# Kernel optimization log

Measured on AMD Instinct MI355X. Metric: run time of the kernel, lower is better.

## Reference

```python
import jax, jax.numpy as jnp
import numpy as np


def _conv1x1_relu(x, W, b):
    # x: (B, Cin, N, k), W: (Cout, Cin), b: (Cout,) -> (B, Cout, N, k)
    return jax.nn.relu(jnp.einsum('bcnk,oc->bonk', x, W) + b[None, :, None, None])


def _knn_idx(pc, k):
    # pc: (B, C, N). Mirrors torch: dis_mat = -||pi - pj||^2, topk (largest) -> nearest.
    G = jnp.einsum('bcn,bcm->bnm', pc, pc)            # (B, N, N)
    sq = jnp.sum(pc * pc, axis=1)                      # (B, N)
    neg_dist = 2.0 * G - sq[:, :, None] - sq[:, None, :]
    _, idx = jax.lax.top_k(neg_dist, k)                # (B, N, k) int32
    return idx


def _group_points(x, idx):
    # x: (B, C, N), idx: (B, N, k) -> (B, C, N, k); out[b,c,n,j] = x[b,c,idx[b,n,j]]
    B, C, N = x.shape
    k = idx.shape[-1]
    idx2 = jnp.broadcast_to(idx.reshape(B, 1, N * k), (B, C, N * k))
    return jnp.take_along_axis(x, idx2, axis=2).reshape(B, C, N, k)


def setup_inputs() -> dict:
    key = jax.random.key(0)
    ks = jax.random.split(key, 8)
    B, N, C, O, K = 8, 4096, 64, 64, 16
    s = 0.05
    return {
        'xyz': jax.random.normal(ks[0], (B, 3, N), dtype=jnp.float32),
        'fea': jax.random.normal(ks[1], (B, C, N), dtype=jnp.float32),
        'Wg1': jax.random.normal(ks[2], (O, 10), dtype=jnp.float32) * s,
        'bg1': jnp.zeros((O,), dtype=jnp.float32),
        'Wg2': jax.random.normal(ks[3], (O, O), dtype=jnp.float32) * s,
        'bg2': jnp.zeros((O,), dtype=jnp.float32),
        'Wf1': jax.random.normal(ks[4], (O, 2 * C), dtype=jnp.float32) * s,
        'bf1': jnp.zeros((O,), dtype=jnp.float32),
        'Wf2': jax.random.normal(ks[5], (O, O), dtype=jnp.float32) * s,
        'bf2': jnp.zeros((O,), dtype=jnp.float32),
        'Wf3': jax.random.normal(ks[6], (O, O), dtype=jnp.float32) * s,
        'bf3': jnp.zeros((O,), dtype=jnp.float32),
        'k': 16,
    }


def reference(xyz, fea, Wg1, bg1, Wg2, bg2, Wf1, bf1, Wf2, bf2, Wf3, bf3, k):
    idx = _knn_idx(fea, k)                             # (B, N, k)

    # get_edge_point: (B, 10, N, k)
    xyz_knn = _group_points(xyz, idx)                  # (B, 3, N, k)
    xyz_c = jnp.broadcast_to(xyz[:, :, :, None], xyz_knn.shape)
    xyz_r = xyz_c - xyz_knn
    xyz_d = jnp.sqrt(jnp.sum(xyz_r * xyz_r, axis=1, keepdims=True))
    geo = jnp.concatenate([xyz_d, xyz_c, xyz_knn, xyz_r], axis=1)

    # get_edge_feature: (B, 2C, N, k)
    fea_knn = _group_points(fea, idx)
    fea_c = jnp.broadcast_to(fea[:, :, :, None], fea_knn.shape)
    edge = jnp.concatenate([fea_c, fea_knn], axis=1)

    g = _conv1x1_relu(geo, Wg1, bg1)
    g = _conv1x1_relu(g, Wg2, bg2)

    f = _conv1x1_relu(edge, Wf1, bf1)
    f = _conv1x1_relu(f, Wf2, bf2)
    f = _conv1x1_relu(f, Wf3, bf3)

    out = jnp.max(g * f, axis=-1)                      # (B, O, N)
    return out
```

## Files before the change

kernel.cpp:

```cpp
#include <hip/hip_runtime.h>
#include <math.h>

#define NB 8
#define NPTS 4096
#define NCH 64
#define NOUT 64
#define KNN 16

#define GLOBAL_AS const __attribute__((address_space(1)))
#define LDS_AS __attribute__((address_space(3)))

#define WS_SQ  0
#define WS_PT  (NB*NPTS)
#define WS_QT  (WS_PT + NB*NPTS*64)
#define WS_IDX (WS_QT + NB*NPTS*64)

__global__ __launch_bounds__(256, 4) void k_knn(const float* __restrict__ fea,
                                                const float* __restrict__ sq,
                                                int* __restrict__ idxout) {
    __shared__ __align__(16) float rowT[64][32];
    __shared__ __align__(16) float colT[2][64 * 64];

    const int b = blockIdx.y;
    const int n0 = blockIdx.x * 32;
    const int tid = threadIdx.x;
    const int lane = tid & 63, w = tid >> 6;
    const int g = lane >> 4, p = lane & 15;
    const int rbase = w * 8 + g * 2;
    const float* feab = fea + (size_t)b * NCH * NPTS;

    auto stage = [&](int buf, int m0) {
#pragma unroll
        for (int i = 0; i < 4; ++i) {
            int k = w * 4 + i;
            int c = 4 * k + (lane >> 4);
            int j = (lane & 15) * 4;
            const float* gp = feab + c * NPTS + m0 + j;
            float* lp = &colT[buf][k * 256];
            __builtin_amdgcn_global_load_lds((GLOBAL_AS void*)gp,
                                             (LDS_AS void*)lp, 16, 0, 0);
        }
    };

#pragma unroll
    for (int i = 0; i < 2; ++i) {
        int e = i * 1024 + tid * 4;
        int c = e >> 5, r = e & 31;
        *(float4*)&rowT[c][r] = *(const float4*)&feab[c * NPTS + n0 + r];
    }

    float lstv[2];
    int   lsti[2];
    float thr[2];
#pragma unroll
    for (int i = 0; i < 2; ++i) {
        lstv[i] = -3.0e38f; lsti[i] = 0; thr[i] = -3.0e38f;
    }

    auto ins = [&](int i, float vv, int col) {
        unsigned long long lt = __ballot(lstv[i] < vv);
        int pos = __popc((unsigned)((lt >> (g * 16)) & 0xFFFFu));
        int nv = __builtin_amdgcn_update_dpp(0, __float_as_int(lstv[i]),
                                             0x101, 0xF, 0xF, true);
        int ni = __builtin_amdgcn_update_dpp(0, lsti[i],
                                             0x101, 0xF, 0xF, true);
        if (p <= pos - 2)      { lstv[i] = __int_as_float(nv); lsti[i] = ni; }
        else if (p == pos - 1) { lstv[i] = vv; lsti[i] = col; }
    };

    stage(0, 0);
    __syncthreads();

    for (int t = 0; t < 64; ++t) {
        const int m0 = t * 64;
        const int cur = t & 1;
        if (t < 63) stage(cur ^ 1, m0 + 64);

        float4 sqc = *(const float4*)&sq[b * NPTS + m0 + p * 4];

        float acc[2][4] = {{0.f,0.f,0.f,0.f},{0.f,0.f,0.f,0.f}};
#pragma unroll 8
        for (int c = 0; c < 64; ++c) {
            float2 rv = *(const float2*)&rowT[c][rbase];
            float4 cv = *(const float4*)&colT[cur][c * 64 + p * 4];
            float cc[4] = {cv.x, cv.y, cv.z, cv.w};
#pragma unroll
            for (int ci = 0; ci < 4; ++ci) {
                acc[0][ci] = fmaf(rv.x, cc[ci], acc[0][ci]);
                acc[1][ci] = fmaf(rv.y, cc[ci], acc[1][ci]);
            }
        }

        float sqa[4] = {sqc.x, sqc.y, sqc.z, sqc.w};
#pragma unroll
        for (int i = 0; i < 2; ++i)
#pragma unroll
            for (int j = 0; j < 4; ++j)
                acc[i][j] = fmaf(2.f, acc[i][j], -sqa[j]);

#pragma unroll
        for (int i = 0; i < 2; ++i) {
            float v0 = acc[i][0], v1 = acc[i][1];
            float v2 = acc[i][2], v3 = acc[i][3];
            float vm = fmaxf(fmaxf(v0, v1), fmaxf(v2, v3));
            unsigned long long bal = __ballot(vm > thr[i]);
            unsigned mg = (unsigned)((bal >> (g * 16)) & 0xFFFFull);
            while (__any(mg != 0u)) {
                bool act = (mg != 0u);
                int srcp = act ? (__ffs(mg) - 1) : 0;
                mg &= (mg - 1u);
                int srcl = (g << 4) | srcp;
                float b0 = __shfl(v0, srcl);
                float b1 = __shfl(v1, srcl);
                float b2 = __shfl(v2, srcl);
                float b3 = __shfl(v3, srcl);
                if (act) {
                    int cb = m0 + srcp * 4;
                    if (b0 > thr[i]) ins(i, b0, cb + 0);
                    if (b1 > thr[i]) ins(i, b1, cb + 1);
                    if (b2 > thr[i]) ins(i, b2, cb + 2);
                    if (b3 > thr[i]) ins(i, b3, cb + 3);
                }
            }
            if (bal) thr[i] = __shfl(lstv[i], 0, 16);
        }
        __syncthreads();
    }

#pragma unroll
    for (int i = 0; i < 2; ++i) {
        int row = rbase + i;
        idxout[((size_t)(b * NPTS) + n0 + row) * KNN + (15 - p)] = lsti[i];
    }
}

__global__ __launch_bounds__(256) void k_pq(const float* __restrict__ fea,
                                            const float* __restrict__ Wf1,
                                            const float* __restrict__ bf1,
                                            float* __restrict__ Pt,
                                            float* __restrict__ Qt,
                                            float* __restrict__ sq) {
    __shared__ __align__(16) float feaT[64][64];
    __shared__ __align__(16) float WT[64][132];
    __shared__ float sb[64];

    const int b = blockIdx.y;
    const int n0 = blockIdx.x * 64;
    const int tid = threadIdx.x;
    const int to = tid & 15, tn = tid >> 4;
    const float* feab = fea + (size_t)b * NCH * NPTS;

#pragma unroll
    for (int i = 0; i < 4; ++i) {
        int e = i * 1024 + tid * 4;
        int c = e >> 6, nn = e & 63;
        *(float4*)&feaT[c][nn] = *(const float4*)&feab[c * NPTS + n0 + nn];
    }
#pragma unroll
    for (int i = 0; i < 8; ++i) {
        int g = tid * 32 + i * 4;
        int op = g >> 6, c = g & 63;
        const float* src = (op < 64) ? &Wf1[op * 128 + c]
                                     : &Wf1[(op - 64) * 128 + 64 + c];
        float4 w = *(const float4*)src;
        WT[c + 0][op] = w.x; WT[c + 1][op] = w.y;
        WT[c + 2][op] = w.z; WT[c + 3][op] = w.w;
    }
    if (tid < 64) sb[tid] = bf1[tid];
    __syncthreads();

    if (tid < 64) {
        float s = 0.f;
#pragma unroll
        for (int c = 0; c < 64; ++c) {
            float v = feaT[c][tid];
            s = fmaf(v, v, s);
        }
        sq[b * NPTS + n0 + tid] = s;
    }

    float acc[4][8];
#pragma unroll
    for (int ni = 0; ni < 4; ++ni)
#pragma unroll
        for (int oj = 0; oj < 8; ++oj) acc[ni][oj] = 0.f;

#pragma unroll 4
    for (int c = 0; c < 64; ++c) {
        float4 a  = *(const float4*)&feaT[c][tn * 4];
        float4 w0 = *(const float4*)&WT[c][to * 8];
        float4 w1 = *(const float4*)&WT[c][to * 8 + 4];
        float av[4] = {a.x, a.y, a.z, a.w};
        float wv[8] = {w0.x, w0.y, w0.z, w0.w, w1.x, w1.y, w1.z, w1.w};
#pragma unroll
        for (int ni = 0; ni < 4; ++ni)
#pragma unroll
            for (int oj = 0; oj < 8; ++oj)
                acc[ni][oj] = fmaf(av[ni], wv[oj], acc[ni][oj]);
    }

    const int opb = to * 8;
#pragma unroll
    for (int ni = 0; ni < 4; ++ni) {
        int n = n0 + tn * 4 + ni;
        size_t base = ((size_t)b * NPTS + n) * 64;
        if (opb < 64) {
            float4 o0, o1;
            o0.x = acc[ni][0] + sb[opb + 0]; o0.y = acc[ni][1] + sb[opb + 1];
            o0.z = acc[ni][2] + sb[opb + 2]; o0.w = acc[ni][3] + sb[opb + 3];
            o1.x = acc[ni][4] + sb[opb + 4]; o1.y = acc[ni][5] + sb[opb + 5];
            o1.z = acc[ni][6] + sb[opb + 6]; o1.w = acc[ni][7] + sb[opb + 7];
            *(float4*)&Pt[base + opb]     = o0;
            *(float4*)&Pt[base + opb + 4] = o1;
        } else {
            float4 o0, o1;
            o0.x = acc[ni][0]; o0.y = acc[ni][1]; o0.z = acc[ni][2]; o0.w = acc[ni][3];
            o1.x = acc[ni][4]; o1.y = acc[ni][5]; o1.z = acc[ni][6]; o1.w = acc[ni][7];
            *(float4*)&Qt[base + opb - 64]     = o0;
            *(float4*)&Qt[base + opb - 64 + 4] = o1;
        }
    }
}

__global__ __launch_bounds__(256) void k_mlp(
    const float* __restrict__ xyz,
    const float* __restrict__ Pt, const float* __restrict__ Qt,
    const int* __restrict__ knnidx,
    const float* __restrict__ Wg1, const float* __restrict__ bg1,
    const float* __restrict__ Wg2, const float* __restrict__ bg2,
    const float* __restrict__ Wf2, const float* __restrict__ bf2,
    const float* __restrict__ Wf3, const float* __restrict__ bf3,
    float* __restrict__ out) {
    __shared__ __align__(16) float bufX[64][68];
    __shared__ __align__(16) float bufY[64][68];
    __shared__ __align__(16) float WbufA[64][68];
    __shared__ __align__(16) float WbufB[64][68];
    __shared__ __align__(16) float geoS[10 * 68];
    __shared__ float biasA[64], biasB[64];
    __shared__ int sidx[64];

    const int b = blockIdx.y;
    const int n0 = blockIdx.x * 4;
    const int tid = threadIdx.x;
    const int to = tid & 15, tp = tid >> 4;

    if (tid < 64)
        sidx[tid] = knnidx[((size_t)(b * NPTS + n0)) * KNN + tid];
    __syncthreads();

    {
        int pair = tid >> 2, q = tid & 3;
        int m = sidx[pair];
        int pt = pair >> 4;
        const float* pB = &Pt[((size_t)b * NPTS + n0 + pt) * 64];
        const float* qB = &Qt[((size_t)b * NPTS + m) * 64];
#pragma unroll
        for (int i = 0; i < 4; ++i) {
            int c0 = q * 16 + i * 4;
            float4 pv = *(const float4*)&pB[c0];
            float4 qv = *(const float4*)&qB[c0];
            bufX[c0 + 0][pair] = fmaxf(pv.x + qv.x, 0.f);
            bufX[c0 + 1][pair] = fmaxf(pv.y + qv.y, 0.f);
            bufX[c0 + 2][pair] = fmaxf(pv.z + qv.z, 0.f);
            bufX[c0 + 3][pair] = fmaxf(pv.w + qv.w, 0.f);
        }
    }
    if (tid < 64) {
        int pair = tid, pt = pair >> 4;
        int m = sidx[pair];
        const float* xb = xyz + (size_t)b * 3 * NPTS;
        float cx = xb[0 * NPTS + n0 + pt], cy = xb[1 * NPTS + n0 + pt], cz = xb[2 * NPTS + n0 + pt];
        float kx = xb[0 * NPTS + m], ky = xb[1 * NPTS + m], kz = xb[2 * NPTS + m];
        float rx = cx - kx, ry = cy - ky, rz = cz - kz;
        float d = sqrtf(rx * rx + ry * ry + rz * rz);
        geoS[0 * 68 + pair] = d;
        geoS[1 * 68 + pair] = cx; geoS[2 * 68 + pair] = cy; geoS[3 * 68 + pair] = cz;
        geoS[4 * 68 + pair] = kx; geoS[5 * 68 + pair] = ky; geoS[6 * 68 + pair] = kz;
        geoS[7 * 68 + pair] = rx; geoS[8 * 68 + pair] = ry; geoS[9 * 68 + pair] = rz;
    }

    auto stageW = [&](const float* W, const float* bv, float (*Wb)[68],
                      float* bias) {
#pragma unroll
        for (int i = 0; i < 4; ++i) {
            int g = tid * 16 + i * 4;
            int o = g >> 6, c = g & 63;
            float4 w = *(const float4*)&W[g];
            Wb[c + 0][o] = w.x; Wb[c + 1][o] = w.y;
            Wb[c + 2][o] = w.z; Wb[c + 3][o] = w.w;
        }
        if (tid < 64) bias[tid] = bv[tid];
    };

    auto gemmPh = [&](const float* src, float* dst, int Kdim,
                      const float (*Wb)[68], const float* bias) {
        float acc[4][4] = {{0.f,0.f,0.f,0.f},{0.f,0.f,0.f,0.f},
                           {0.f,0.f,0.f,0.f},{0.f,0.f,0.f,0.f}};
#pragma unroll 2
        for (int c = 0; c < Kdim; ++c) {
            float4 w = *(const float4*)&Wb[c][tp * 4];
            float4 a = *(const float4*)(src + c * 68 + to * 4);
            float wr[4] = {w.x, w.y, w.z, w.w};
            float ar[4] = {a.x, a.y, a.z, a.w};
#pragma unroll
            for (int oi = 0; oi < 4; ++oi)
#pragma unroll
                for (int pj = 0; pj < 4; ++pj)
                    acc[oi][pj] = fmaf(wr[oi], ar[pj], acc[oi][pj]);
        }
#pragma unroll
        for (int oi = 0; oi < 4; ++oi) {
            float bo = bias[tp * 4 + oi];
            float4 o4;
            o4.x = fmaxf(acc[oi][0] + bo, 0.f);
            o4.y = fmaxf(acc[oi][1] + bo, 0.f);
            o4.z = fmaxf(acc[oi][2] + bo, 0.f);
            o4.w = fmaxf(acc[oi][3] + bo, 0.f);
            *(float4*)(dst + (tp * 4 + oi) * 68 + to * 4) = o4;
        }
    };

    stageW(Wf2, bf2, WbufA, biasA);
    stageW(Wf3, bf3, WbufB, biasB);
    __syncthreads();

    gemmPh(&bufX[0][0], &bufY[0][0], 64, WbufA, biasA);
    __syncthreads();

    float f3r[4][4];
    {
        float acc[4][4] = {{0.f,0.f,0.f,0.f},{0.f,0.f,0.f,0.f},
                           {0.f,0.f,0.f,0.f},{0.f,0.f,0.f,0.f}};
#pragma unroll 2
        for (int c = 0; c < 64; ++c) {
            float4 w = *(const float4*)&WbufB[c][tp * 4];
            float4 a = *(const float4*)&bufY[c][to * 4];
            float wr[4] = {w.x, w.y, w.z, w.w};
            float ar[4] = {a.x, a.y, a.z, a.w};
#pragma unroll
            for (int oi = 0; oi < 4; ++oi)
#pragma unroll
                for (int pj = 0; pj < 4; ++pj)
                    acc[oi][pj] = fmaf(wr[oi], ar[pj], acc[oi][pj]);
        }
#pragma unroll
        for (int oi = 0; oi < 4; ++oi) {
            float bo = biasB[tp * 4 + oi];
            f3r[oi][0] = fmaxf(acc[oi][0] + bo, 0.f);
            f3r[oi][1] = fmaxf(acc[oi][1] + bo, 0.f);
            f3r[oi][2] = fmaxf(acc[oi][2] + bo, 0.f);
            f3r[oi][3] = fmaxf(acc[oi][3] + bo, 0.f);
        }
    }
    {
        for (int e = tid; e < 640; e += 256) {
            int o = e / 10, c = e - o * 10;
            WbufA[c][o] = Wg1[e];
        }
        if (tid < 64) biasA[tid] = bg1[tid];
    }
    __syncthreads();

    gemmPh(geoS, &bufY[0][0], 10, WbufA, biasA);
    stageW(Wg2, bg2, WbufB, biasB);
    __syncthreads();

    {
        float acc[4][4] = {{0.f,0.f,0.f,0.f},{0.f,0.f,0.f,0.f},
                           {0.f,0.f,0.f,0.f},{0.f,0.f,0.f,0.f}};
#pragma unroll 2
        for (int c = 0; c < 64; ++c) {
            float4 w = *(const float4*)&WbufB[c][tp * 4];
            float4 a = *(const float4*)&bufY[c][to * 4];
            float wr[4] = {w.x, w.y, w.z, w.w};
            float ar[4] = {a.x, a.y, a.z, a.w};
#pragma unroll
            for (int oi = 0; oi < 4; ++oi)
#pragma unroll
                for (int pj = 0; pj < 4; ++pj)
                    acc[oi][pj] = fmaf(wr[oi], ar[pj], acc[oi][pj]);
        }
        float mx[4];
#pragma unroll
        for (int oi = 0; oi < 4; ++oi) {
            float bo = biasB[tp * 4 + oi];
            float m0_ = fmaxf(acc[oi][0] + bo, 0.f) * f3r[oi][0];
            float m1_ = fmaxf(acc[oi][1] + bo, 0.f) * f3r[oi][1];
            float m2_ = fmaxf(acc[oi][2] + bo, 0.f) * f3r[oi][2];
            float m3_ = fmaxf(acc[oi][3] + bo, 0.f) * f3r[oi][3];
            mx[oi] = fmaxf(fmaxf(m0_, m1_), fmaxf(m2_, m3_));
        }
#pragma unroll
        for (int oi = 0; oi < 4; ++oi) {
            mx[oi] = fmaxf(mx[oi], __shfl_xor(mx[oi], 1));
            mx[oi] = fmaxf(mx[oi], __shfl_xor(mx[oi], 2));
        }
        if ((to & 3) == 0) {
            int pt = to >> 2;
#pragma unroll
            for (int oi = 0; oi < 4; ++oi) {
                int o = tp * 4 + oi;
                out[((size_t)b * 64 + o) * NPTS + n0 + pt] = mx[oi];
            }
        }
    }
}

extern "C" void kernel_launch(void* const* d_in, const int* in_sizes, int n_in,
                              void* d_out, int out_size, void* d_ws, size_t ws_size,
                              hipStream_t stream) {
    const float* xyz = (const float*)d_in[0];
    const float* fea = (const float*)d_in[1];
    const float* Wg1 = (const float*)d_in[2];
    const float* bg1 = (const float*)d_in[3];
    const float* Wg2 = (const float*)d_in[4];
    const float* bg2 = (const float*)d_in[5];
    const float* Wf1 = (const float*)d_in[6];
    const float* bf1 = (const float*)d_in[7];
    const float* Wf2 = (const float*)d_in[8];
    const float* bf2 = (const float*)d_in[9];
    const float* Wf3 = (const float*)d_in[10];
    const float* bf3 = (const float*)d_in[11];
    float* out = (float*)d_out;
    float* ws = (float*)d_ws;

    float* sq = ws + WS_SQ;
    float* Pt = ws + WS_PT;
    float* Qt = ws + WS_QT;
    int* idxw = (int*)(ws + WS_IDX);

    k_pq  <<<dim3(64, 8),    dim3(256), 0, stream>>>(fea, Wf1, bf1, Pt, Qt, sq);
    k_knn <<<dim3(128, 8),   dim3(256), 0, stream>>>(fea, sq, idxw);
    k_mlp <<<dim3(1024, 8),  dim3(256), 0, stream>>>(xyz, Pt, Qt, idxw,
                                                     Wg1, bg1, Wg2, bg2,
                                                     Wf2, bf2, Wf3, bf3, out);
}
```

Before: 622.3 us.

## Split KNN candidate scan into two halves and merge top-k in MLP kernel

The KNN kernel now splits the 4096 candidate columns into two halves across a new grid dimension, doubling block count, and writes per-half top-16 values and 16-bit indices. The MLP kernel merges the two sorted lists by rank counting in shared memory before gathering. The KNN column staging drops from double buffering to a single LDS buffer with an extra barrier, which cuts LDS use to allow more resident blocks. The cost is extra workspace traffic for values, a merge step in the MLP kernel, and less overlap of loads with compute.

```diff
diff --git a/kernel.cpp b/kernel.cpp
--- a/kernel.cpp
+++ b/kernel.cpp
@@ -6,6 +6,7 @@
 #define NCH 64
 #define NOUT 64
 #define KNN 16
+#define HALFC 2048
 
 #define GLOBAL_AS const __attribute__((address_space(1)))
 #define LDS_AS __attribute__((address_space(3)))
@@ -13,30 +14,122 @@
 #define WS_SQ  0
 #define WS_PT  (NB*NPTS)
 #define WS_QT  (WS_PT + NB*NPTS*64)
-#define WS_IDX (WS_QT + NB*NPTS*64)
-
-__global__ __launch_bounds__(256, 4) void k_knn(const float* __restrict__ fea,
+#define WS_VH  (WS_QT + NB*NPTS*64)
+#define WS_IH  (WS_VH + NB*NPTS*32)
+
+__global__ __launch_bounds__(256) void k_pq(const float* __restrict__ fea,
+                                            const float* __restrict__ Wf1,
+                                            const float* __restrict__ bf1,
+                                            float* __restrict__ Pt,
+                                            float* __restrict__ Qt,
+                                            float* __restrict__ sq) {
+    __shared__ __align__(16) float feaT[64][64];
+    __shared__ __align__(16) float WT[64][132];
+    __shared__ float sb[64];
+
+    const int b = blockIdx.y;
+    const int n0 = blockIdx.x * 64;
+    const int tid = threadIdx.x;
+    const int to = tid & 15, tn = tid >> 4;
+    const float* feab = fea + (size_t)b * NCH * NPTS;
+
+#pragma unroll
+    for (int i = 0; i < 4; ++i) {
+        int e = i * 1024 + tid * 4;
+        int c = e >> 6, nn = e & 63;
+        *(float4*)&feaT[c][nn] = *(const float4*)&feab[c * NPTS + n0 + nn];
+    }
+#pragma unroll
+    for (int i = 0; i < 8; ++i) {
+        int g = tid * 32 + i * 4;
+        int op = g >> 6, c = g & 63;
+        const float* src = (op < 64) ? &Wf1[op * 128 + c]
+                                     : &Wf1[(op - 64) * 128 + 64 + c];
+        float4 w = *(const float4*)src;
+        WT[c + 0][op] = w.x; WT[c + 1][op] = w.y;
+        WT[c + 2][op] = w.z; WT[c + 3][op] = w.w;
+    }
+    if (tid < 64) sb[tid] = bf1[tid];
+    __syncthreads();
+
+    if (tid < 64) {
+        float s = 0.f;
+#pragma unroll
+        for (int c = 0; c < 64; ++c) {
+            float v = feaT[c][tid];
+            s = fmaf(v, v, s);
+        }
+        sq[b * NPTS + n0 + tid] = s;
+    }
+
+    float acc[4][8];
+#pragma unroll
+    for (int ni = 0; ni < 4; ++ni)
+#pragma unroll
+        for (int oj = 0; oj < 8; ++oj) acc[ni][oj] = 0.f;
+
+#pragma unroll 4
+    for (int c = 0; c < 64; ++c) {
+        float4 a  = *(const float4*)&feaT[c][tn * 4];
+        float4 w0 = *(const float4*)&WT[c][to * 8];
+        float4 w1 = *(const float4*)&WT[c][to * 8 + 4];
+        float av[4] = {a.x, a.y, a.z, a.w};
+        float wv[8] = {w0.x, w0.y, w0.z, w0.w, w1.x, w1.y, w1.z, w1.w};
+#pragma unroll
+        for (int ni = 0; ni < 4; ++ni)
+#pragma unroll
+            for (int oj = 0; oj < 8; ++oj)
+                acc[ni][oj] = fmaf(av[ni], wv[oj], acc[ni][oj]);
+    }
+
+    const int opb = to * 8;
+#pragma unroll
+    for (int ni = 0; ni < 4; ++ni) {
+        int n = n0 + tn * 4 + ni;
+        size_t base = ((size_t)b * NPTS + n) * 64;
+        if (opb < 64) {
+            float4 o0, o1;
+            o0.x = acc[ni][0] + sb[opb + 0]; o0.y = acc[ni][1] + sb[opb + 1];
+            o0.z = acc[ni][2] + sb[opb + 2]; o0.w = acc[ni][3] + sb[opb + 3];
+            o1.x = acc[ni][4] + sb[opb + 4]; o1.y = acc[ni][5] + sb[opb + 5];
+            o1.z = acc[ni][6] + sb[opb + 6]; o1.w = acc[ni][7] + sb[opb + 7];
+            *(float4*)&Pt[base + opb]     = o0;
+            *(float4*)&Pt[base + opb + 4] = o1;
+        } else {
+            float4 o0, o1;
+            o0.x = acc[ni][0]; o0.y = acc[ni][1]; o0.z = acc[ni][2]; o0.w = acc[ni][3];
+            o1.x = acc[ni][4]; o1.y = acc[ni][5]; o1.z = acc[ni][6]; o1.w = acc[ni][7];
+            *(float4*)&Qt[base + opb - 64]     = o0;
+            *(float4*)&Qt[base + opb - 64 + 4] = o1;
+        }
+    }
+}
+
+__global__ __launch_bounds__(256, 6) void k_knn(const float* __restrict__ fea,
                                                 const float* __restrict__ sq,
-                                                int* __restrict__ idxout) {
+                                                float* __restrict__ vh,
+                                                unsigned short* __restrict__ ih) {
     __shared__ __align__(16) float rowT[64][32];
-    __shared__ __align__(16) float colT[2][64 * 64];
-
-    const int b = blockIdx.y;
+    __shared__ __align__(16) float colT[64 * 64];
+
+    const int b = blockIdx.z;
+    const int half = blockIdx.y;
     const int n0 = blockIdx.x * 32;
+    const int cbase = half * HALFC;
     const int tid = threadIdx.x;
     const int lane = tid & 63, w = tid >> 6;
     const int g = lane >> 4, p = lane & 15;
     const int rbase = w * 8 + g * 2;
     const float* feab = fea + (size_t)b * NCH * NPTS;
 
-    auto stage = [&](int buf, int m0) {
+    auto stage = [&](int m0) {
 #pragma unroll
         for (int i = 0; i < 4; ++i) {
             int k = w * 4 + i;
             int c = 4 * k + (lane >> 4);
             int j = (lane & 15) * 4;
             const float* gp = feab + c * NPTS + m0 + j;
-            float* lp = &colT[buf][k * 256];
+            float* lp = &colT[k * 256];
             __builtin_amdgcn_global_load_lds((GLOBAL_AS void*)gp,
                                              (LDS_AS void*)lp, 16, 0, 0);
         }
@@ -68,13 +161,11 @@
         else if (p == pos - 1) { lstv[i] = vv; lsti[i] = col; }
     };
 
-    stage(0, 0);
-    __syncthreads();
-
-    for (int t = 0; t < 64; ++t) {
-        const int m0 = t * 64;
-        const int cur = t & 1;
-        if (t < 63) stage(cur ^ 1, m0 + 64);
+    stage(cbase);
+    __syncthreads();
+
+    for (int t = 0; t < 32; ++t) {
+        const int m0 = cbase + t * 64;
 
         float4 sqc = *(const float4*)&sq[b * NPTS + m0 + p * 4];
 
@@ -82,7 +173,7 @@
 #pragma unroll 8
         for (int c = 0; c < 64; ++c) {
             float2 rv = *(const float2*)&rowT[c][rbase];
-            float4 cv = *(const float4*)&colT[cur][c * 64 + p * 4];
+            float4 cv = *(const float4*)&colT[c * 64 + p * 4];
             float cc[4] = {cv.x, cv.y, cv.z, cv.w};
 #pragma unroll
             for (int ci = 0; ci < 4; ++ci) {
@@ -90,6 +181,9 @@
                 acc[1][ci] = fmaf(rv.y, cc[ci], acc[1][ci]);
             }
         }
+
+        __syncthreads();
+        if (t < 31) stage(m0 + 64);
 
         float sqa[4] = {sqc.x, sqc.y, sqc.z, sqc.w};
 #pragma unroll
@@ -130,102 +224,16 @@
 #pragma unroll
     for (int i = 0; i < 2; ++i) {
         int row = rbase + i;
-        idxout[((size_t)(b * NPTS) + n0 + row) * KNN + (15 - p)] = lsti[i];
-    }
-}
-
-__global__ __launch_bounds__(256) void k_pq(const float* __restrict__ fea,
-                                            const float* __restrict__ Wf1,
-                                            const float* __restrict__ bf1,
-                                            float* __restrict__ Pt,
-                                            float* __restrict__ Qt,
-                                            float* __restrict__ sq) {
-    __shared__ __align__(16) float feaT[64][64];
-    __shared__ __align__(16) float WT[64][132];
-    __shared__ float sb[64];
-
-    const int b = blockIdx.y;
-    const int n0 = blockIdx.x * 64;
-    const int tid = threadIdx.x;
-    const int to = tid & 15, tn = tid >> 4;
-    const float* feab = fea + (size_t)b * NCH * NPTS;
-
-#pragma unroll
-    for (int i = 0; i < 4; ++i) {
-        int e = i * 1024 + tid * 4;
-        int c = e >> 6, nn = e & 63;
-        *(float4*)&feaT[c][nn] = *(const float4*)&feab[c * NPTS + n0 + nn];
-    }
-#pragma unroll
-    for (int i = 0; i < 8; ++i) {
-        int g = tid * 32 + i * 4;
-        int op = g >> 6, c = g & 63;
-        const float* src = (op < 64) ? &Wf1[op * 128 + c]
-                                     : &Wf1[(op - 64) * 128 + 64 + c];
-        float4 w = *(const float4*)src;
-        WT[c + 0][op] = w.x; WT[c + 1][op] = w.y;
-        WT[c + 2][op] = w.z; WT[c + 3][op] = w.w;
-    }
-    if (tid < 64) sb[tid] = bf1[tid];
-    __syncthreads();
-
-    if (tid < 64) {
-        float s = 0.f;
-#pragma unroll
-        for (int c = 0; c < 64; ++c) {
-            float v = feaT[c][tid];
-            s = fmaf(v, v, s);
-        }
-        sq[b * NPTS + n0 + tid] = s;
-    }
-
-    float acc[4][8];
-#pragma unroll
-    for (int ni = 0; ni < 4; ++ni)
-#pragma unroll
-        for (int oj = 0; oj < 8; ++oj) acc[ni][oj] = 0.f;
-
-#pragma unroll 4
-    for (int c = 0; c < 64; ++c) {
-        float4 a  = *(const float4*)&feaT[c][tn * 4];
-        float4 w0 = *(const float4*)&WT[c][to * 8];
-        float4 w1 = *(const float4*)&WT[c][to * 8 + 4];
-        float av[4] = {a.x, a.y, a.z, a.w};
-        float wv[8] = {w0.x, w0.y, w0.z, w0.w, w1.x, w1.y, w1.z, w1.w};
-#pragma unroll
-        for (int ni = 0; ni < 4; ++ni)
-#pragma unroll
-            for (int oj = 0; oj < 8; ++oj)
-                acc[ni][oj] = fmaf(av[ni], wv[oj], acc[ni][oj]);
-    }
-
-    const int opb = to * 8;
-#pragma unroll
-    for (int ni = 0; ni < 4; ++ni) {
-        int n = n0 + tn * 4 + ni;
-        size_t base = ((size_t)b * NPTS + n) * 64;
-        if (opb < 64) {
-            float4 o0, o1;
-            o0.x = acc[ni][0] + sb[opb + 0]; o0.y = acc[ni][1] + sb[opb + 1];
-            o0.z = acc[ni][2] + sb[opb + 2]; o0.w = acc[ni][3] + sb[opb + 3];
-            o1.x = acc[ni][4] + sb[opb + 4]; o1.y = acc[ni][5] + sb[opb + 5];
-            o1.z = acc[ni][6] + sb[opb + 6]; o1.w = acc[ni][7] + sb[opb + 7];
-            *(float4*)&Pt[base + opb]     = o0;
-            *(float4*)&Pt[base + opb + 4] = o1;
-        } else {
-            float4 o0, o1;
-            o0.x = acc[ni][0]; o0.y = acc[ni][1]; o0.z = acc[ni][2]; o0.w = acc[ni][3];
-            o1.x = acc[ni][4]; o1.y = acc[ni][5]; o1.z = acc[ni][6]; o1.w = acc[ni][7];
-            *(float4*)&Qt[base + opb - 64]     = o0;
-            *(float4*)&Qt[base + opb - 64 + 4] = o1;
-        }
+        size_t base = ((size_t)(b * NPTS) + n0 + row) * 32 + half * 16;
+        vh[base + (15 - p)] = lstv[i];
+        ih[base + (15 - p)] = (unsigned short)lsti[i];
     }
 }
 
 __global__ __launch_bounds__(256) void k_mlp(
     const float* __restrict__ xyz,
     const float* __restrict__ Pt, const float* __restrict__ Qt,
-    const int* __restrict__ knnidx,
+    const float* __restrict__ vh, const unsigned short* __restrict__ ih,
     const float* __restrict__ Wg1, const float* __restrict__ bg1,
     const float* __restrict__ Wg2, const float* __restrict__ bg2,
     const float* __restrict__ Wf2, const float* __restrict__ bf2,
@@ -236,6 +244,8 @@
     __shared__ __align__(16) float WbufA[64][68];
     __shared__ __align__(16) float WbufB[64][68];
     __shared__ __align__(16) float geoS[10 * 68];
+    __shared__ float vbuf[4][32];
+    __shared__ unsigned short ibuf[4][32];
     __shared__ float biasA[64], biasB[64];
     __shared__ int sidx[64];
 
@@ -244,8 +254,30 @@
     const int tid = threadIdx.x;
     const int to = tid & 15, tp = tid >> 4;
 
-    if (tid < 64)
-        sidx[tid] = knnidx[((size_t)(b * NPTS + n0)) * KNN + tid];
+    if (tid < 128) {
+        int r = tid >> 5, e = tid & 31;
+        size_t row = (size_t)(b * NPTS) + n0 + r;
+        vbuf[r][e] = vh[row * 32 + e];
+        ibuf[r][e] = ih[row * 32 + e];
+    }
+    __syncthreads();
+    if (tid < 128) {
+        int r = tid >> 5, e = tid & 31;
+        float myv = vbuf[r][e];
+        int rank;
+        if (e < 16) {
+            int cnt = 0;
+#pragma unroll
+            for (int k = 0; k < 16; ++k) cnt += (vbuf[r][16 + k] > myv);
+            rank = e + cnt;
+        } else {
+            int cnt = 0;
+#pragma unroll
+            for (int k = 0; k < 16; ++k) cnt += (vbuf[r][k] >= myv);
+            rank = (e - 16) + cnt;
+        }
+        if (rank < 16) sidx[r * 16 + rank] = (int)ibuf[r][e];
+    }
     __syncthreads();
 
     {
@@ -427,11 +459,12 @@
     float* sq = ws + WS_SQ;
     float* Pt = ws + WS_PT;
     float* Qt = ws + WS_QT;
-    int* idxw = (int*)(ws + WS_IDX);
-
-    k_pq  <<<dim3(64, 8),    dim3(256), 0, stream>>>(fea, Wf1, bf1, Pt, Qt, sq);
-    k_knn <<<dim3(128, 8),   dim3(256), 0, stream>>>(fea, sq, idxw);
-    k_mlp <<<dim3(1024, 8),  dim3(256), 0, stream>>>(xyz, Pt, Qt, idxw,
-                                                     Wg1, bg1, Wg2, bg2,
-                                                     Wf2, bf2, Wf3, bf3, out);
+    float* vh = ws + WS_VH;
+    unsigned short* ih = (unsigned short*)(ws + WS_IH);
+
+    k_pq  <<<dim3(64, 8),     dim3(256), 0, stream>>>(fea, Wf1, bf1, Pt, Qt, sq);
+    k_knn <<<dim3(128, 2, 8), dim3(256), 0, stream>>>(fea, sq, vh, ih);
+    k_mlp <<<dim3(1024, 8),   dim3(256), 0, stream>>>(xyz, Pt, Qt, vh, ih,
+                                                      Wg1, bg1, Wg2, bg2,
+                                                      Wf2, bf2, Wf3, bf3, out);
 }
```

New measurement: 686.6 us. 1.1x slower.
